# Kernel optimization log

Measured on AMD Instinct MI355X. Metric: run time of the kernel, lower is better.

Reference implementation:

```python
import jax, jax.numpy as jnp
import numpy as np

NU, NI, D, E = 100000, 50000, 128, 800000

FLOAT_NAMES = ["emb_user", "emb_item"]
for _l in (1, 2):
    FLOAT_NAMES += [f"l{_l}_ui_pW1", f"l{_l}_ui_pb1", f"l{_l}_ui_pW2", f"l{_l}_ui_pb2"]
    for _e in ("ui", "iu"):
        FLOAT_NAMES += [f"l{_l}_{_e}_Wn", f"l{_l}_{_e}_bn", f"l{_l}_{_e}_Ws", f"l{_l}_{_e}_bs"]
FLOAT_NAMES += ["head_W", "head_b"]


def setup_inputs() -> dict:
    key = jax.random.key(0)
    shapes = {"emb_user": (NU, D), "emb_item": (NI, D), "head_W": (1, D), "head_b": (1,)}
    for n in FLOAT_NAMES:
        if n not in shapes:
            shapes[n] = (D, D) if n.endswith(("W1", "W2", "Wn", "Ws")) else (D,)
    inp = {}
    for i, n in enumerate(FLOAT_NAMES):
        inp[n] = jax.random.normal(jax.random.fold_in(key, i), shapes[n], jnp.float32) * 0.05
    inp["ue_src"] = jax.random.randint(jax.random.fold_in(key, 100), (E,), 0, NU)
    inp["ue_dst"] = jax.random.randint(jax.random.fold_in(key, 101), (E,), 0, NI)
    inp["iu_src"] = jax.random.randint(jax.random.fold_in(key, 102), (E,), 0, NI)
    inp["iu_dst"] = jax.random.randint(jax.random.fold_in(key, 103), (E,), 0, NU)
    inp["num_user"] = NU
    inp["num_item"] = NI
    return inp


def _scatter_mean(src, idx, n):
    # sum per segment / clamped count  (matches torch scatter_add_ + clamp(min=1))
    s = jax.ops.segment_sum(src, idx, num_segments=n)
    c = jax.ops.segment_sum(jnp.ones((src.shape[0],), src.dtype), idx, num_segments=n)
    return s / jnp.maximum(c, 1.0)[:, None]


def _forward(p, ue_src, ue_dst, iu_src, iu_dst, nu, ni):
    # hidden_dim == EMBED_DIM -> no input_proj, just ReLU on embedding tables
    xu = jax.nn.relu(p["emb_user"])  # [NU, D]
    xi = jax.nn.relu(p["emb_item"])  # [NI, D]
    for l in (1, 2):
        # PRMPSAGEConv: user -> item (item=dst predicts user/src features, aggregate residuals)
        h = jax.nn.relu(xi @ p[f"l{l}_ui_pW1"].T + p[f"l{l}_ui_pb1"])
        pred = h @ p[f"l{l}_ui_pW2"].T + p[f"l{l}_ui_pb2"]           # [NI, D]
        resid = xu[ue_src] - pred[ue_dst]                              # [E, D]
        agg_i = _scatter_mean(resid, ue_dst, ni)                       # [NI, D]
        out_i = (agg_i @ p[f"l{l}_ui_Wn"].T + p[f"l{l}_ui_bn"]
                 + xi @ p[f"l{l}_ui_Ws"].T + p[f"l{l}_ui_bs"])
        # BipartiteSAGEConv: item -> user (mean-aggregate src feats)
        agg_u = _scatter_mean(xi[iu_src], iu_dst, nu)                  # [NU, D]
        out_u = (agg_u @ p[f"l{l}_iu_Wn"].T + p[f"l{l}_iu_bn"]
                 + xu @ p[f"l{l}_iu_Ws"].T + p[f"l{l}_iu_bs"])
        # dropout is identity in eval; ReLU after each layer per original forward
        xu, xi = jax.nn.relu(out_u), jax.nn.relu(out_i)
    return (xu @ p["head_W"].T + p["head_b"])[:, 0]  # squeeze(-1) -> [NU]


def reference(emb_user, emb_item,
              l1_ui_pW1, l1_ui_pb1, l1_ui_pW2, l1_ui_pb2,
              l1_ui_Wn, l1_ui_bn, l1_ui_Ws, l1_ui_bs,
              l1_iu_Wn, l1_iu_bn, l1_iu_Ws, l1_iu_bs,
              l2_ui_pW1, l2_ui_pb1, l2_ui_pW2, l2_ui_pb2,
              l2_ui_Wn, l2_ui_bn, l2_ui_Ws, l2_ui_bs,
              l2_iu_Wn, l2_iu_bn, l2_iu_Ws, l2_iu_bs,
              head_W, head_b,
              ue_src, ue_dst, iu_src, iu_dst, num_user, num_item):
    floats = (emb_user, emb_item,
              l1_ui_pW1, l1_ui_pb1, l1_ui_pW2, l1_ui_pb2,
              l1_ui_Wn, l1_ui_bn, l1_ui_Ws, l1_ui_bs,
              l1_iu_Wn, l1_iu_bn, l1_iu_Ws, l1_iu_bs,
              l2_ui_pW1, l2_ui_pb1, l2_ui_pW2, l2_ui_pb2,
              l2_ui_Wn, l2_ui_bn, l2_ui_Ws, l2_ui_bs,
              l2_iu_Wn, l2_iu_bn, l2_iu_Ws, l2_iu_bs,
              head_W, head_b)
    p = dict(zip(FLOAT_NAMES, floats))
    return _forward(p, ue_src, ue_dst, iu_src, iu_dst, num_user, num_item)
```

## Files before the change

kernel.cpp:

```cpp
#include <hip/hip_runtime.h>
#include <hip/hip_bf16.h>

#define DD 128
#define PAD_I 64
#define PAD_U 48

typedef __attribute__((ext_vector_type(8))) short bf16x8;
typedef __attribute__((ext_vector_type(4))) float f32x4;

__device__ __forceinline__ unsigned short rne_bf16(float x) {
    unsigned int u = __float_as_uint(x);
    return (unsigned short)((u + 0x7FFFu + ((u >> 16) & 1u)) >> 16);
}

template <bool R>
__device__ __forceinline__ void load_split8(const float* __restrict__ p,
                                            bf16x8& hf, bf16x8& lf) {
    float4 v0 = *reinterpret_cast<const float4*>(p);
    float4 v1 = *reinterpret_cast<const float4*>(p + 4);
    float x[8] = {v0.x, v0.y, v0.z, v0.w, v1.x, v1.y, v1.z, v1.w};
#pragma unroll
    for (int j = 0; j < 8; j += 2) {
        float a = R ? fmaxf(x[j], 0.f) : x[j];
        float b = R ? fmaxf(x[j + 1], 0.f) : x[j + 1];
        __hip_bfloat162 h2 = __float22bfloat162_rn(make_float2(a, b));
        float2 hr = __bfloat1622float2(h2);
        __hip_bfloat162 l2 = __float22bfloat162_rn(make_float2(a - hr.x, b - hr.y));
        hf[j]     = (short)__bfloat16_as_ushort(h2.x);
        hf[j + 1] = (short)__bfloat16_as_ushort(h2.y);
        lf[j]     = (short)__bfloat16_as_ushort(l2.x);
        lf[j + 1] = (short)__bfloat16_as_ushort(l2.y);
    }
}


__global__ __launch_bounds__(256) void zeroi_k(int* __restrict__ p, int n) {
    int gid = blockIdx.x * 256 + threadIdx.x;
    if (gid < n) p[gid] = 0;
}

__global__ __launch_bounds__(256) void fill_k(const int* __restrict__ src,
                                              const int* __restrict__ dst,
                                              int* __restrict__ cur,
                                              int* __restrict__ pad, int PAD, int E) {
    int e = blockIdx.x * 256 + threadIdx.x;
    if (e >= E) return;
    int d = dst[e];
    int slot = atomicAdd(&cur[d], 1);
    if (slot < PAD) pad[(size_t)d * PAD + slot] = src[e];
}

template <bool RELU>
__device__ __forceinline__ void gather_body(const float* __restrict__ feat,
                                            const int* __restrict__ cur,
                                            const int* __restrict__ pad, int PAD,
                                            float* __restrict__ out, int N, int blk) {
    int row = blk * 4 + (threadIdx.x >> 6);
    if (row >= N) return;
    int lane = threadIdx.x & 63;
    int p = lane >> 4, c = lane & 15;
    int deg = cur[row]; if (deg > PAD) deg = PAD;
    const int* pl = pad + (size_t)row * PAD;

    float4 a0 = make_float4(0.f, 0.f, 0.f, 0.f);
    float4 a1 = make_float4(0.f, 0.f, 0.f, 0.f);
    float4 b0 = make_float4(0.f, 0.f, 0.f, 0.f);
    float4 b1 = make_float4(0.f, 0.f, 0.f, 0.f);
    int j = p;
    for (; j + 4 < deg; j += 8) {
        int s0 = pl[j];
        int s1 = pl[j + 4];
        const float* q0 = feat + (size_t)s0 * DD + c * 8;
        const float* q1 = feat + (size_t)s1 * DD + c * 8;
        float4 u0 = *reinterpret_cast<const float4*>(q0);
        float4 u1 = *reinterpret_cast<const float4*>(q0 + 4);
        float4 u2 = *reinterpret_cast<const float4*>(q1);
        float4 u3 = *reinterpret_cast<const float4*>(q1 + 4);
        if (RELU) {
            u0.x = fmaxf(u0.x, 0.f); u0.y = fmaxf(u0.y, 0.f); u0.z = fmaxf(u0.z, 0.f); u0.w = fmaxf(u0.w, 0.f);
            u1.x = fmaxf(u1.x, 0.f); u1.y = fmaxf(u1.y, 0.f); u1.z = fmaxf(u1.z, 0.f); u1.w = fmaxf(u1.w, 0.f);
            u2.x = fmaxf(u2.x, 0.f); u2.y = fmaxf(u2.y, 0.f); u2.z = fmaxf(u2.z, 0.f); u2.w = fmaxf(u2.w, 0.f);
            u3.x = fmaxf(u3.x, 0.f); u3.y = fmaxf(u3.y, 0.f); u3.z = fmaxf(u3.z, 0.f); u3.w = fmaxf(u3.w, 0.f);
        }
        a0.x += u0.x; a0.y += u0.y; a0.z += u0.z; a0.w += u0.w;
        a1.x += u1.x; a1.y += u1.y; a1.z += u1.z; a1.w += u1.w;
        b0.x += u2.x; b0.y += u2.y; b0.z += u2.z; b0.w += u2.w;
        b1.x += u3.x; b1.y += u3.y; b1.z += u3.z; b1.w += u3.w;
    }
    if (j < deg) {
        int s = pl[j];
        const float* q = feat + (size_t)s * DD + c * 8;
        float4 u0 = *reinterpret_cast<const float4*>(q);
        float4 u1 = *reinterpret_cast<const float4*>(q + 4);
        if (RELU) {
            u0.x = fmaxf(u0.x, 0.f); u0.y = fmaxf(u0.y, 0.f); u0.z = fmaxf(u0.z, 0.f); u0.w = fmaxf(u0.w, 0.f);
            u1.x = fmaxf(u1.x, 0.f); u1.y = fmaxf(u1.y, 0.f); u1.z = fmaxf(u1.z, 0.f); u1.w = fmaxf(u1.w, 0.f);
        }
        a0.x += u0.x; a0.y += u0.y; a0.z += u0.z; a0.w += u0.w;
        a1.x += u1.x; a1.y += u1.y; a1.z += u1.z; a1.w += u1.w;
    }
    a0.x += b0.x; a0.y += b0.y; a0.z += b0.z; a0.w += b0.w;
    a1.x += b1.x; a1.y += b1.y; a1.z += b1.z; a1.w += b1.w;

#pragma unroll
    for (int off = 16; off <= 32; off <<= 1) {
        a0.x += __shfl_xor(a0.x, off); a0.y += __shfl_xor(a0.y, off);
        a0.z += __shfl_xor(a0.z, off); a0.w += __shfl_xor(a0.w, off);
        a1.x += __shfl_xor(a1.x, off); a1.y += __shfl_xor(a1.y, off);
        a1.z += __shfl_xor(a1.z, off); a1.w += __shfl_xor(a1.w, off);
    }
    if (p == 0) {
        float iv = 1.0f / (float)(deg > 1 ? deg : 1);
        a0.x *= iv; a0.y *= iv; a0.z *= iv; a0.w *= iv;
        a1.x *= iv; a1.y *= iv; a1.z *= iv; a1.w *= iv;
        float* o = out + (size_t)row * DD + c * 8;
        *reinterpret_cast<float4*>(o) = a0;
        *reinterpret_cast<float4*>(o + 4) = a1;
    }
}

template <bool RELU>
__global__ __launch_bounds__(256) void gather_mean_k(const float* __restrict__ feat,
                                                     const int* __restrict__ cur,
                                                     const int* __restrict__ pad, int PAD,
                                                     float* __restrict__ out, int N) {
    gather_body<RELU>(feat, cur, pad, PAD, out, N, blockIdx.x);
}

template <bool RELU1, bool RELU2>
__global__ __launch_bounds__(256) void gather2_k(
        const float* __restrict__ feat1, const int* __restrict__ cur1,
        const int* __restrict__ pad1, int PAD1, float* __restrict__ out1, int N1, int nb1,
        const float* __restrict__ feat2, const int* __restrict__ cur2,
        const int* __restrict__ pad2, int PAD2, float* __restrict__ out2, int N2, int nb2) {
    int b = blockIdx.x;
    int which, idx;
    if (nb2 == 2 * nb1) {
        int tri = b / 3, rem = b - tri * 3;
        if (rem == 0) { which = 0; idx = tri; }
        else          { which = 1; idx = 2 * tri + rem - 1; }
    } else {
        which = (b < nb1) ? 0 : 1;
        idx = which ? (b - nb1) : b;
    }
    if (which == 0) gather_body<RELU1>(feat1, cur1, pad1, PAD1, out1, N1, idx);
    else            gather_body<RELU2>(feat2, cur2, pad2, PAD2, out2, N2, idx);
}


struct W12 { const float* p[12]; };

__global__ __launch_bounds__(256) void wsplit_k(W12 ws, unsigned short* __restrict__ hi,
                                                unsigned short* __restrict__ lo) {
    int idx = blockIdx.x * 256 + threadIdx.x;
    if (idx >= 12 * DD * DD) return;
    int m = idx >> 14, pk = idx & 16383;
    int j = pk & 7, lane = (pk >> 3) & 63, t = (pk >> 9) & 7, kc = (pk >> 12) & 3;
    int src = (t * 16 + (lane & 15)) * DD + kc * 32 + (lane >> 4) * 8 + j;
    float x = ws.p[m][src];
    unsigned short h = rne_bf16(x);
    float r = x - __uint_as_float((unsigned int)h << 16);
    hi[idx] = h;
    lo[idx] = rne_bf16(r);
}


template <bool RELX>
__global__ __launch_bounds__(256) void fused23_k(
        const float* __restrict__ X,
        const unsigned short* __restrict__ W1h, const unsigned short* __restrict__ W1l,
        const float* __restrict__ B1,
        const unsigned short* __restrict__ W2h, const unsigned short* __restrict__ W2l,
        const float* __restrict__ B2,
        float* __restrict__ Io, int N, const int* __restrict__ deg) {
    __shared__ __align__(16) float hl[64][DD + 4];

    const int tid = threadIdx.x;
    const int w = tid >> 6, l = tid & 63;
    const int l15 = l & 15, lq = l >> 4;

    const int rowA = blockIdx.x * 64 + w * 16 + l15;
    const int rA = rowA < N ? rowA : N - 1;
    const float* xp = X + (size_t)rA * DD;

    bf16x8 ah[4], al[4];
#pragma unroll
    for (int kc = 0; kc < 4; ++kc)
        load_split8<RELX>(xp + kc * 32 + lq * 8, ah[kc], al[kc]);

    f32x4 acc[8];
#pragma unroll
    for (int t = 0; t < 8; ++t) acc[t] = (f32x4){0.f, 0.f, 0.f, 0.f};

#pragma unroll
    for (int kc = 0; kc < 4; ++kc) {
        const size_t fb = ((size_t)(kc * 8) * 64 + l) * 8;
        bf16x8 bh[8], bl[8];
#pragma unroll
        for (int t = 0; t < 8; ++t) bh[t] = *reinterpret_cast<const bf16x8*>(W1h + fb + t * 512);
#pragma unroll
        for (int t = 0; t < 8; ++t) bl[t] = *reinterpret_cast<const bf16x8*>(W1l + fb + t * 512);
#pragma unroll
        for (int t = 0; t < 8; ++t)
            acc[t] = __builtin_amdgcn_mfma_f32_16x16x32_bf16(ah[kc], bh[t], acc[t], 0, 0, 0);
#pragma unroll
        for (int t = 0; t < 8; ++t)
            acc[t] = __builtin_amdgcn_mfma_f32_16x16x32_bf16(al[kc], bh[t], acc[t], 0, 0, 0);
#pragma unroll
        for (int t = 0; t < 8; ++t)
            acc[t] = __builtin_amdgcn_mfma_f32_16x16x32_bf16(ah[kc], bl[t], acc[t], 0, 0, 0);
    }

    const int lr0 = w * 16 + lq * 4;
#pragma unroll
    for (int t = 0; t < 8; ++t) {
        const int col = t * 16 + l15;
        const float b = B1[col];
#pragma unroll
        for (int r = 0; r < 4; ++r)
            hl[lr0 + r][col] = fmaxf(acc[t][r] + b, 0.f);
    }
    __syncthreads();

    bf16x8 ah2[4], al2[4];
#pragma unroll
    for (int kc = 0; kc < 4; ++kc)
        load_split8<false>(&hl[w * 16 + l15][kc * 32 + lq * 8], ah2[kc], al2[kc]);

#pragma unroll
    for (int t = 0; t < 8; ++t) acc[t] = (f32x4){0.f, 0.f, 0.f, 0.f};

#pragma unroll
    for (int kc = 0; kc < 4; ++kc) {
        const size_t fb = ((size_t)(kc * 8) * 64 + l) * 8;
        bf16x8 bh[8], bl[8];
#pragma unroll
        for (int t = 0; t < 8; ++t) bh[t] = *reinterpret_cast<const bf16x8*>(W2h + fb + t * 512);
#pragma unroll
        for (int t = 0; t < 8; ++t) bl[t] = *reinterpret_cast<const bf16x8*>(W2l + fb + t * 512);
#pragma unroll
        for (int t = 0; t < 8; ++t)
            acc[t] = __builtin_amdgcn_mfma_f32_16x16x32_bf16(ah2[kc], bh[t], acc[t], 0, 0, 0);
#pragma unroll
        for (int t = 0; t < 8; ++t)
            acc[t] = __builtin_amdgcn_mfma_f32_16x16x32_bf16(al2[kc], bh[t], acc[t], 0, 0, 0);
#pragma unroll
        for (int t = 0; t < 8; ++t)
            acc[t] = __builtin_amdgcn_mfma_f32_16x16x32_bf16(ah2[kc], bl[t], acc[t], 0, 0, 0);
    }

    const int orow0 = blockIdx.x * 64 + w * 16 + lq * 4;
#pragma unroll
    for (int t = 0; t < 8; ++t) {
        const int col = t * 16 + l15;
        const float b2v = B2[col];
#pragma unroll
        for (int r = 0; r < 4; ++r) {
            const int grow = orow0 + r;
            if (grow >= N) continue;
            float fl = deg[grow] > 0 ? 1.f : 0.f;
            float* op = Io + (size_t)grow * DD + col;
            *op = *op - (acc[t][r] + b2v) * fl;
        }
    }
}

template <bool RELX2>
__device__ __forceinline__ void dual_acc(
        const float* __restrict__ X1,
        const unsigned short* __restrict__ W1h, const unsigned short* __restrict__ W1l,
        const float* __restrict__ X2,
        const unsigned short* __restrict__ W2h, const unsigned short* __restrict__ W2l,
        int N, int base, int l, int lq, int l15, f32x4 (&acc)[2][8]) {
    int rA[2];
#pragma unroll
    for (int g = 0; g < 2; ++g) {
        int r = base + g * 16 + l15;
        rA[g] = r < N ? r : N - 1;
    }
    {
        bf16x8 ah[2][4], al[2][4];
#pragma unroll
        for (int g = 0; g < 2; ++g)
#pragma unroll
            for (int kc = 0; kc < 4; ++kc)
                load_split8<false>(X1 + (size_t)rA[g] * DD + kc * 32 + lq * 8, ah[g][kc], al[g][kc]);
#pragma unroll
        for (int kc = 0; kc < 4; ++kc) {
            const size_t fb = ((size_t)(kc * 8) * 64 + l) * 8;
            bf16x8 bh[8], bl[8];
#pragma unroll
            for (int t = 0; t < 8; ++t) bh[t] = *reinterpret_cast<const bf16x8*>(W1h + fb + t * 512);
#pragma unroll
            for (int t = 0; t < 8; ++t) bl[t] = *reinterpret_cast<const bf16x8*>(W1l + fb + t * 512);
#pragma unroll
            for (int g = 0; g < 2; ++g) {
#pragma unroll
                for (int t = 0; t < 8; ++t)
                    acc[g][t] = __builtin_amdgcn_mfma_f32_16x16x32_bf16(ah[g][kc], bh[t], acc[g][t], 0, 0, 0);
#pragma unroll
                for (int t = 0; t < 8; ++t)
                    acc[g][t] = __builtin_amdgcn_mfma_f32_16x16x32_bf16(al[g][kc], bh[t], acc[g][t], 0, 0, 0);
#pragma unroll
                for (int t = 0; t < 8; ++t)
                    acc[g][t] = __builtin_amdgcn_mfma_f32_16x16x32_bf16(ah[g][kc], bl[t], acc[g][t], 0, 0, 0);
            }
        }
    }
    {
        bf16x8 ah[2][4], al[2][4];
#pragma unroll
        for (int g = 0; g < 2; ++g)
#pragma unroll
            for (int kc = 0; kc < 4; ++kc)
                load_split8<RELX2>(X2 + (size_t)rA[g] * DD + kc * 32 + lq * 8, ah[g][kc], al[g][kc]);
#pragma unroll
        for (int kc = 0; kc < 4; ++kc) {
            const size_t fb = ((size_t)(kc * 8) * 64 + l) * 8;
            bf16x8 bh[8], bl[8];
#pragma unroll
            for (int t = 0; t < 8; ++t) bh[t] = *reinterpret_cast<const bf16x8*>(W2h + fb + t * 512);
#pragma unroll
            for (int t = 0; t < 8; ++t) bl[t] = *reinterpret_cast<const bf16x8*>(W2l + fb + t * 512);
#pragma unroll
            for (int g = 0; g < 2; ++g) {
#pragma unroll
                for (int t = 0; t < 8; ++t)
                    acc[g][t] = __builtin_amdgcn_mfma_f32_16x16x32_bf16(ah[g][kc], bh[t], acc[g][t], 0, 0, 0);
#pragma unroll
                for (int t = 0; t < 8; ++t)
                    acc[g][t] = __builtin_amdgcn_mfma_f32_16x16x32_bf16(al[g][kc], bh[t], acc[g][t], 0, 0, 0);
#pragma unroll
                for (int t = 0; t < 8; ++t)
                    acc[g][t] = __builtin_amdgcn_mfma_f32_16x16x32_bf16(ah[g][kc], bl[t], acc[g][t], 0, 0, 0);
            }
        }
    }
}

template <bool RELX2>
__global__ __launch_bounds__(256) void gemm_dual_k(
        const float* __restrict__ X1,
        const unsigned short* __restrict__ W1h, const unsigned short* __restrict__ W1l,
        const float* __restrict__ B1,
        const float* __restrict__ X2,
        const unsigned short* __restrict__ W2h, const unsigned short* __restrict__ W2l,
        const float* __restrict__ B2,
        float* __restrict__ out, int N) {
    const int tid = threadIdx.x;
    const int w = tid >> 6, l = tid & 63;
    const int l15 = l & 15, lq = l >> 4;
    const int base = blockIdx.x * 128 + w * 32;

    f32x4 acc[2][8];
#pragma unroll
    for (int g = 0; g < 2; ++g)
#pragma unroll
        for (int t = 0; t < 8; ++t) acc[g][t] = (f32x4){0.f, 0.f, 0.f, 0.f};

    dual_acc<RELX2>(X1, W1h, W1l, X2, W2h, W2l, N, base, l, lq, l15, acc);

#pragma unroll
    for (int g = 0; g < 2; ++g)
#pragma unroll
        for (int t = 0; t < 8; ++t) {
            const int col = t * 16 + l15;
            const float bias = B1[col] + B2[col];
#pragma unroll
            for (int r = 0; r < 4; ++r) {
                const int grow = base + g * 16 + lq * 4 + r;
                if (grow >= N) continue;
                out[(size_t)grow * DD + col] = fmaxf(acc[g][t][r] + bias, 0.f);
            }
        }
}

template <bool RELX2>
__global__ __launch_bounds__(256) void gemm_dual_head_k(
        const float* __restrict__ X1,
        const unsigned short* __restrict__ W1h, const unsigned short* __restrict__ W1l,
        const float* __restrict__ B1,
        const float* __restrict__ X2,
        const unsigned short* __restrict__ W2h, const unsigned short* __restrict__ W2l,
        const float* __restrict__ B2,
        const float* __restrict__ hW, const float* __restrict__ hb,
        float* __restrict__ out, int N) {
    const int tid = threadIdx.x;
    const int w = tid >> 6, l = tid & 63;
    const int l15 = l & 15, lq = l >> 4;
    const int base = blockIdx.x * 128 + w * 32;

    f32x4 acc[2][8];
#pragma unroll
    for (int g = 0; g < 2; ++g)
#pragma unroll
        for (int t = 0; t < 8; ++t) acc[g][t] = (f32x4){0.f, 0.f, 0.f, 0.f};

    dual_acc<RELX2>(X1, W1h, W1l, X2, W2h, W2l, N, base, l, lq, l15, acc);

    float hwv[8], bv[8];
#pragma unroll
    for (int t = 0; t < 8; ++t) {
        const int col = t * 16 + l15;
        hwv[t] = hW[col];
        bv[t]  = B1[col] + B2[col];
    }
    const float hb0 = hb[0];

#pragma unroll
    for (int g = 0; g < 2; ++g)
#pragma unroll
        for (int r = 0; r < 4; ++r) {
            float s = 0.f;
#pragma unroll
            for (int t = 0; t < 8; ++t)
                s += fmaxf(acc[g][t][r] + bv[t], 0.f) * hwv[t];
            s += __shfl_xor(s, 1);
            s += __shfl_xor(s, 2);
            s += __shfl_xor(s, 4);
            s += __shfl_xor(s, 8);
            const int grow = base + g * 16 + lq * 4 + r;
            if (l15 == 0 && grow < N) out[grow] = s + hb0;
        }
}


extern "C" void kernel_launch(void* const* d_in, const int* in_sizes, int n_in,
                              void* d_out, int out_size, void* d_ws, size_t ws_size,
                              hipStream_t stream) {
    const float* emb_user = (const float*)d_in[0];
    const float* emb_item = (const float*)d_in[1];
    const float* head_W   = (const float*)d_in[26];
    const float* head_b   = (const float*)d_in[27];
    const int*   ue_src   = (const int*)d_in[28];
    const int*   ue_dst   = (const int*)d_in[29];
    const int*   iu_src   = (const int*)d_in[30];
    const int*   iu_dst   = (const int*)d_in[31];

    const int NU = in_sizes[0] / DD;
    const int NI = in_sizes[1] / DD;
    const int E  = in_sizes[28];

    const float* L[2][12];
    for (int l = 0; l < 2; ++l)
        for (int j = 0; j < 12; ++j) L[l][j] = (const float*)d_in[2 + l * 12 + j];

    const size_t SU = (size_t)NU * DD, SI = (size_t)NI * DD;
    const size_t WPLANE = 12 * (size_t)DD * DD;
    size_t need = 0;
    auto pad256 = [](size_t b) { return (b + 255) & ~(size_t)255; };
    need += 2 * pad256(SU * 4) + pad256(SI * 4);
    need += pad256((size_t)NI * 4) + pad256((size_t)NU * 4);
    need += pad256((size_t)NI * PAD_I * 4) + pad256((size_t)NU * PAD_U * 4);
    need += 2 * pad256(WPLANE * 2);
    if (ws_size < need) return;

    char* w = (char*)d_ws;
    auto alloc = [&](size_t bytes) { void* p = w; w += pad256(bytes); return p; };
    float* Ua    = (float*)alloc(SU * 4);
    float* Ub    = (float*)alloc(SU * 4);
    float* Ia    = (float*)alloc(SI * 4);
    int*   deg_i = (int*)alloc((size_t)NI * 4);
    int*   deg_u = (int*)alloc((size_t)NU * 4);
    int*   adj_i = (int*)alloc((size_t)NI * PAD_I * 4);
    int*   adj_u = (int*)alloc((size_t)NU * PAD_U * 4);
    unsigned short* Whi = (unsigned short*)alloc(WPLANE * 2);
    unsigned short* Wlo = (unsigned short*)alloc(WPLANE * 2);

    auto cdiv = [](long long a, long long b) { return (int)((a + b - 1) / b); };

    W12 ws;
    for (int l = 0; l < 2; ++l) {
        ws.p[l * 6 + 0] = L[l][0];
        ws.p[l * 6 + 1] = L[l][2];
        ws.p[l * 6 + 2] = L[l][4];
        ws.p[l * 6 + 3] = L[l][6];
        ws.p[l * 6 + 4] = L[l][8];
        ws.p[l * 6 + 5] = L[l][10];
    }
    wsplit_k<<<cdiv(WPLANE, 256), 256, 0, stream>>>(ws, Whi, Wlo);

    zeroi_k<<<cdiv(NI, 256), 256, 0, stream>>>(deg_i, NI);
    zeroi_k<<<cdiv(NU, 256), 256, 0, stream>>>(deg_u, NU);
    fill_k<<<cdiv(E, 256), 256, 0, stream>>>(ue_src, ue_dst, deg_i, adj_i, PAD_I, E);
    fill_k<<<cdiv(E, 256), 256, 0, stream>>>(iu_src, iu_dst, deg_u, adj_u, PAD_U, E);

    const int gI64 = cdiv(NI, 64);
    const int gI128 = cdiv(NI, 128), gU128 = cdiv(NU, 128);
    const int nbI = cdiv(NI, 4), nbU = cdiv(NU, 4);
    const size_t WM = (size_t)DD * DD;
    auto WH = [&](int l, int m) { return Whi + ((size_t)l * 6 + m) * WM; };
    auto WL = [&](int l, int m) { return Wlo + ((size_t)l * 6 + m) * WM; };

    gather2_k<true, true><<<nbI + nbU, 256, 0, stream>>>(
        emb_user, deg_i, adj_i, PAD_I, Ia, NI, nbI,
        emb_item, deg_u, adj_u, PAD_U, Ua, NU, nbU);
    gemm_dual_k<true><<<gU128, 256, 0, stream>>>(Ua, WH(0,4), WL(0,4), L[0][9],
                                                 emb_user, WH(0,5), WL(0,5), L[0][11], Ua, NU);
    fused23_k<true><<<gI64, 256, 0, stream>>>(emb_item, WH(0,0), WL(0,0), L[0][1],
                                              WH(0,1), WL(0,1), L[0][3], Ia, NI, deg_i);
    gemm_dual_k<true><<<gI128, 256, 0, stream>>>(Ia, WH(0,2), WL(0,2), L[0][5],
                                                 emb_item, WH(0,3), WL(0,3), L[0][7], Ia, NI);

    gather_mean_k<false><<<nbU, 256, 0, stream>>>(Ia, deg_u, adj_u, PAD_U, Ub, NU);
    gemm_dual_head_k<false><<<gU128, 256, 0, stream>>>(
        Ub, WH(1,4), WL(1,4), L[1][9],
        Ua, WH(1,5), WL(1,5), L[1][11],
        head_W, head_b, (float*)d_out, NU);
}
```

Before: 416.9 us.

## Fuse item predictor MLP and neighbor/self GEMMs into one kernel

Merges the two-stage predictor MLP kernel and the following dual neighbor/self GEMM for the item side into a single kernel. The residual aggregate is formed in shared memory and fed straight into the Wn GEMM, and the already-split X fragments are reused for the Ws GEMM. This removes one launch and a full write and re-read of the item aggregate buffer. In exchange, each block does more sequential MFMA work with extra syncs, at 64-row tiles instead of 128.

Result: faster. 398.6 us (-4.4%).

```diff
diff --git a/kernel.cpp b/kernel.cpp
--- a/kernel.cpp
+++ b/kernel.cpp
@@ -32,6 +32,23 @@
         lf[j + 1] = (short)__bfloat16_as_ushort(l2.y);
     }
 }
+
+#define STAGE_MFMA(AH, AL, WH_, WL_, ACC)                                               \
+    _Pragma("unroll")                                                                   \
+    for (int kc = 0; kc < 4; ++kc) {                                                    \
+        const size_t fb = ((size_t)(kc * 8) * 64 + l) * 8;                              \
+        bf16x8 bh[8], bl[8];                                                            \
+        _Pragma("unroll") for (int t = 0; t < 8; ++t)                                   \
+            bh[t] = *reinterpret_cast<const bf16x8*>((WH_) + fb + t * 512);             \
+        _Pragma("unroll") for (int t = 0; t < 8; ++t)                                   \
+            bl[t] = *reinterpret_cast<const bf16x8*>((WL_) + fb + t * 512);             \
+        _Pragma("unroll") for (int t = 0; t < 8; ++t)                                   \
+            ACC[t] = __builtin_amdgcn_mfma_f32_16x16x32_bf16(AH[kc], bh[t], ACC[t], 0, 0, 0); \
+        _Pragma("unroll") for (int t = 0; t < 8; ++t)                                   \
+            ACC[t] = __builtin_amdgcn_mfma_f32_16x16x32_bf16(AL[kc], bh[t], ACC[t], 0, 0, 0); \
+        _Pragma("unroll") for (int t = 0; t < 8; ++t)                                   \
+            ACC[t] = __builtin_amdgcn_mfma_f32_16x16x32_bf16(AH[kc], bl[t], ACC[t], 0, 0, 0); \
+    }
 
 
 __global__ __launch_bounds__(256) void zeroi_k(int* __restrict__ p, int n) {
@@ -166,13 +183,17 @@
 
 
 template <bool RELX>
-__global__ __launch_bounds__(256) void fused23_k(
+__global__ __launch_bounds__(256) void item1_k(
         const float* __restrict__ X,
-        const unsigned short* __restrict__ W1h, const unsigned short* __restrict__ W1l,
-        const float* __restrict__ B1,
-        const unsigned short* __restrict__ W2h, const unsigned short* __restrict__ W2l,
-        const float* __restrict__ B2,
-        float* __restrict__ Io, int N, const int* __restrict__ deg) {
+        const unsigned short* __restrict__ P1h, const unsigned short* __restrict__ P1l,
+        const float* __restrict__ pb1,
+        const unsigned short* __restrict__ P2h, const unsigned short* __restrict__ P2l,
+        const float* __restrict__ pb2,
+        const unsigned short* __restrict__ Nh,  const unsigned short* __restrict__ Nl,
+        const float* __restrict__ bn,
+        const unsigned short* __restrict__ Sh,  const unsigned short* __restrict__ Sl,
+        const float* __restrict__ bs,
+        float* __restrict__ Ia, int N, const int* __restrict__ deg) {
     __shared__ __align__(16) float hl[64][DD + 4];
 
     const int tid = threadIdx.x;
@@ -183,84 +204,72 @@
     const int rA = rowA < N ? rowA : N - 1;
     const float* xp = X + (size_t)rA * DD;
 
-    bf16x8 ah[4], al[4];
+    bf16x8 axh[4], axl[4];
 #pragma unroll
     for (int kc = 0; kc < 4; ++kc)
-        load_split8<RELX>(xp + kc * 32 + lq * 8, ah[kc], al[kc]);
+        load_split8<RELX>(xp + kc * 32 + lq * 8, axh[kc], axl[kc]);
 
     f32x4 acc[8];
 #pragma unroll
     for (int t = 0; t < 8; ++t) acc[t] = (f32x4){0.f, 0.f, 0.f, 0.f};
 
-#pragma unroll
-    for (int kc = 0; kc < 4; ++kc) {
-        const size_t fb = ((size_t)(kc * 8) * 64 + l) * 8;
-        bf16x8 bh[8], bl[8];
-#pragma unroll
-        for (int t = 0; t < 8; ++t) bh[t] = *reinterpret_cast<const bf16x8*>(W1h + fb + t * 512);
-#pragma unroll
-        for (int t = 0; t < 8; ++t) bl[t] = *reinterpret_cast<const bf16x8*>(W1l + fb + t * 512);
-#pragma unroll
-        for (int t = 0; t < 8; ++t)
-            acc[t] = __builtin_amdgcn_mfma_f32_16x16x32_bf16(ah[kc], bh[t], acc[t], 0, 0, 0);
-#pragma unroll
-        for (int t = 0; t < 8; ++t)
-            acc[t] = __builtin_amdgcn_mfma_f32_16x16x32_bf16(al[kc], bh[t], acc[t], 0, 0, 0);
-#pragma unroll
-        for (int t = 0; t < 8; ++t)
-            acc[t] = __builtin_amdgcn_mfma_f32_16x16x32_bf16(ah[kc], bl[t], acc[t], 0, 0, 0);
-    }
+    STAGE_MFMA(axh, axl, P1h, P1l, acc)
 
     const int lr0 = w * 16 + lq * 4;
 #pragma unroll
     for (int t = 0; t < 8; ++t) {
         const int col = t * 16 + l15;
-        const float b = B1[col];
+        const float b = pb1[col];
 #pragma unroll
         for (int r = 0; r < 4; ++r)
             hl[lr0 + r][col] = fmaxf(acc[t][r] + b, 0.f);
     }
     __syncthreads();
 
-    bf16x8 ah2[4], al2[4];
+    bf16x8 ahh[4], ahl[4];
 #pragma unroll
     for (int kc = 0; kc < 4; ++kc)
-        load_split8<false>(&hl[w * 16 + l15][kc * 32 + lq * 8], ah2[kc], al2[kc]);
+        load_split8<false>(&hl[w * 16 + l15][kc * 32 + lq * 8], ahh[kc], ahl[kc]);
+    __syncthreads();
 
 #pragma unroll
     for (int t = 0; t < 8; ++t) acc[t] = (f32x4){0.f, 0.f, 0.f, 0.f};
-
-#pragma unroll
-    for (int kc = 0; kc < 4; ++kc) {
-        const size_t fb = ((size_t)(kc * 8) * 64 + l) * 8;
-        bf16x8 bh[8], bl[8];
-#pragma unroll
-        for (int t = 0; t < 8; ++t) bh[t] = *reinterpret_cast<const bf16x8*>(W2h + fb + t * 512);
-#pragma unroll
-        for (int t = 0; t < 8; ++t) bl[t] = *reinterpret_cast<const bf16x8*>(W2l + fb + t * 512);
-#pragma unroll
-        for (int t = 0; t < 8; ++t)
-            acc[t] = __builtin_amdgcn_mfma_f32_16x16x32_bf16(ah2[kc], bh[t], acc[t], 0, 0, 0);
-#pragma unroll
-        for (int t = 0; t < 8; ++t)
-            acc[t] = __builtin_amdgcn_mfma_f32_16x16x32_bf16(al2[kc], bh[t], acc[t], 0, 0, 0);
-#pragma unroll
-        for (int t = 0; t < 8; ++t)
-            acc[t] = __builtin_amdgcn_mfma_f32_16x16x32_bf16(ah2[kc], bl[t], acc[t], 0, 0, 0);
-    }
-
-    const int orow0 = blockIdx.x * 64 + w * 16 + lq * 4;
+    STAGE_MFMA(ahh, ahl, P2h, P2l, acc)
+
 #pragma unroll
     for (int t = 0; t < 8; ++t) {
         const int col = t * 16 + l15;
-        const float b2v = B2[col];
+        const float b2v = pb2[col];
 #pragma unroll
         for (int r = 0; r < 4; ++r) {
-            const int grow = orow0 + r;
+            const int grow = blockIdx.x * 64 + lr0 + r;
+            const int gr = grow < N ? grow : N - 1;
+            float fl = deg[gr] > 0 ? 1.f : 0.f;
+            float ag = Ia[(size_t)gr * DD + col];
+            hl[lr0 + r][col] = ag - (acc[t][r] + b2v) * fl;
+        }
+    }
+    __syncthreads();
+
+    bf16x8 avh[4], avl[4];
+#pragma unroll
+    for (int kc = 0; kc < 4; ++kc)
+        load_split8<false>(&hl[w * 16 + l15][kc * 32 + lq * 8], avh[kc], avl[kc]);
+
+#pragma unroll
+    for (int t = 0; t < 8; ++t) acc[t] = (f32x4){0.f, 0.f, 0.f, 0.f};
+    STAGE_MFMA(avh, avl, Nh, Nl, acc)
+    STAGE_MFMA(axh, axl, Sh, Sl, acc)
+
+#pragma unroll
+    for (int t = 0; t < 8; ++t) {
+        const int col = t * 16 + l15;
+        const float bias = bn[col] + bs[col];
+#pragma unroll
+        for (int r = 0; r < 4; ++r) {
+            const int grow = blockIdx.x * 64 + lr0 + r;
             if (grow >= N) continue;
-            float fl = deg[grow] > 0 ? 1.f : 0.f;
-            float* op = Io + (size_t)grow * DD + col;
-            *op = *op - (acc[t][r] + b2v) * fl;
+            Ia[(size_t)grow * DD + col] = fmaxf(acc[t][r] + bias, 0.f);
         }
     }
 }
@@ -491,16 +500,20 @@
     const size_t WM = (size_t)DD * DD;
     auto WH = [&](int l, int m) { return Whi + ((size_t)l * 6 + m) * WM; };
     auto WL = [&](int l, int m) { return Wlo + ((size_t)l * 6 + m) * WM; };
+    (void)gI128;
 
     gather2_k<true, true><<<nbI + nbU, 256, 0, stream>>>(
         emb_user, deg_i, adj_i, PAD_I, Ia, NI, nbI,
         emb_item, deg_u, adj_u, PAD_U, Ua, NU, nbU);
     gemm_dual_k<true><<<gU128, 256, 0, stream>>>(Ua, WH(0,4), WL(0,4), L[0][9],
                                                  emb_user, WH(0,5), WL(0,5), L[0][11], Ua, NU);
-    fused23_k<true><<<gI64, 256, 0, stream>>>(emb_item, WH(0,0), WL(0,0), L[0][1],
-                                              WH(0,1), WL(0,1), L[0][3], Ia, NI, deg_i);
-    gemm_dual_k<true><<<gI128, 256, 0, stream>>>(Ia, WH(0,2), WL(0,2), L[0][5],
-                                                 emb_item, WH(0,3), WL(0,3), L[0][7], Ia, NI);
+    item1_k<true><<<gI64, 256, 0, stream>>>(
+        emb_item,
+        WH(0,0), WL(0,0), L[0][1],
+        WH(0,1), WL(0,1), L[0][3],
+        WH(0,2), WL(0,2), L[0][5],
+        WH(0,3), WL(0,3), L[0][7],
+        Ia, NI, deg_i);
 
     gather_mean_k<false><<<nbU, 256, 0, stream>>>(Ia, deg_u, adj_u, PAD_U, Ub, NU);
     gemm_dual_head_k<false><<<gU128, 256, 0, stream>>>(
```
